# Optimization experiments

Hardware: AMD Instinct MI355X
Metric: run time of the kernel (lower is better)

## Reference

```python
import jax, jax.numpy as jnp
import numpy as np

S = 1024      # flattened hierarchical sequence length
D = 1024      # n_embd
H = 16        # n_head
HD = D // H   # head dim (64)
NL = 6        # n_layer
DFF = 4 * D
EPS = 1.1920929e-07  # torch rms_norm default eps (float32 machine eps)


def setup_inputs() -> dict:
    key = jax.random.key(0)
    ks = jax.random.split(key, 12)
    s = 0.02
    return {
        "x": jax.random.normal(ks[0], (1, S, D), jnp.float32),
        "Wq": jax.random.normal(ks[1], (NL, D, D), jnp.float32) * s,
        "Wk": jax.random.normal(ks[2], (NL, D, D), jnp.float32) * s,
        "Wv": jax.random.normal(ks[3], (NL, D, D), jnp.float32) * s,
        "Wo": jax.random.normal(ks[4], (NL, D, D), jnp.float32) * s,
        "lamb": jnp.full((NL,), 0.5, jnp.float32),
        "lambdas": jnp.tile(jnp.array([1.0, 0.0], jnp.float32), (NL, 1)),
        "Wfc": jax.random.normal(ks[5], (NL, DFF, D), jnp.float32) * s,
        "Wp": jax.random.normal(ks[6], (NL, D, DFF), jnp.float32) * s,
        "levels": jax.random.randint(ks[7], (S,), 0, 3, jnp.int32),
        "sample_idx": jnp.sort(jax.random.randint(ks[8], (S,), 0, 8, jnp.int32)),
    }


def rms(t):
    return t * jax.lax.rsqrt(jnp.mean(t * t, axis=-1, keepdims=True) + EPS)


def rope(t):
    # t: [B, T, H, hd]; torch-style half-split rotary
    hd = t.shape[-1]
    d = hd // 2
    inv = 1.0 / (10000.0 ** (jnp.arange(0, hd, 2, dtype=jnp.float32) / hd))
    fr = jnp.outer(jnp.arange(t.shape[1], dtype=jnp.float32), inv)  # [T, d]
    cos = jnp.cos(fr)[None, :, None, :]
    sin = jnp.sin(fr)[None, :, None, :]
    x1, x2 = t[..., :d], t[..., d:]
    return jnp.concatenate([x1 * cos + x2 * sin, -x1 * sin + x2 * cos], axis=-1)


def markov_mask(levels, sample_idx):
    # allowed(q,kv) = causal & same-sample & NOT(levels[kv]==0 and a level-0
    # token exists strictly between kv and q). Equivalent to the torch
    # markov_causal_mask, computed via a cumsum instead of torch.any.
    n = levels.shape[0]
    pos = jnp.arange(n)
    causal = pos[:, None] >= pos[None, :]
    same = sample_idx[:, None] == sample_idx[None, :]
    c = jnp.cumsum((levels == 0).astype(jnp.int32))
    cpad = jnp.concatenate([jnp.zeros((1,), jnp.int32), c])  # cpad[i]=#l0 in [0,i)
    # count of level-0 tokens at positions p with kv < p < q
    cnt = cpad[pos[:, None]] - cpad[pos[None, :] + 1]
    markov = (levels[None, :] == 0) & (cnt > 0)
    return causal & same & ~markov


def reference(x, Wq, Wk, Wv, Wo, lamb, lambdas, Wfc, Wp, levels, sample_idx):
    mask = markov_mask(levels, sample_idx)[None, None]  # [1,1,S,S]
    scale = HD ** -0.5
    neg = jnp.float32(-1e30)

    x = rms(x)          # norm of the hierarchical-trajectory embedding
    x0 = x
    v1 = None
    for i in range(NL):
        xl = lambdas[i, 0] * x + lambdas[i, 1] * x0
        xn = rms(xl)
        B, T = xn.shape[0], xn.shape[1]
        q = (xn @ Wq[i].T).reshape(B, T, H, HD)
        k = (xn @ Wk[i].T).reshape(B, T, H, HD)
        v = (xn @ Wv[i].T).reshape(B, T, H, HD)
        if v1 is None:
            v1 = v
        v = (1.0 - lamb[i]) * v + lamb[i] * v1   # value residual
        q, k = rms(q), rms(k)                    # QK RMSNorm
        q, k = rope(q), rope(k)
        scores = jnp.einsum("bqhd,bkhd->bhqk", q, k) * scale
        scores = jnp.where(mask, scores, neg)
        p = jax.nn.softmax(scores, axis=-1)
        y = jnp.einsum("bhqk,bkhd->bqhd", p, v).reshape(B, T, D)
        x = xl + y @ Wo[i].T
        h = rms(x) @ Wfc[i].T
        h = jnp.square(jax.nn.relu(h))           # relu(x)^2 activation
        x = x + h @ Wp[i].T
    return rms(x)
```

## Files before the change

kernel.cpp:

```cpp
#include <hip/hip_runtime.h>

#define SQ 1024
#define DM 1024
#define NH 16
#define HD 64
#define NL 6
#define DFF 4096
#define EPS 1.1920929e-07f

typedef __attribute__((ext_vector_type(8))) short short8;
typedef __attribute__((ext_vector_type(4))) float floatx4;
typedef __attribute__((address_space(1))) const unsigned int GU32;
typedef __attribute__((address_space(3))) unsigned int LU32;

__device__ __forceinline__ unsigned short f2b(float f) {
    union { float f; unsigned int u; } x; x.f = f;
    unsigned int r = x.u + 0x7fffu + ((x.u >> 16) & 1u);
    return (unsigned short)(r >> 16);
}

__device__ __forceinline__ float wsum(float v) {
#pragma unroll
    for (int m = 32; m >= 1; m >>= 1) v += __shfl_xor(v, m, 64);
    return v;
}
__device__ __forceinline__ float bsum(float v) {
    __shared__ float sh[4];
    v = wsum(v);
    __syncthreads();
    if ((threadIdx.x & 63) == 0) sh[threadIdx.x >> 6] = v;
    __syncthreads();
    return sh[0] + sh[1] + sh[2] + sh[3];
}

__global__ void convert_all(const float* __restrict__ s0, const float* __restrict__ s1,
                            const float* __restrict__ s2, const float* __restrict__ s3,
                            const float* __restrict__ s4, const float* __restrict__ s5,
                            unsigned short* __restrict__ d0, unsigned short* __restrict__ d1,
                            unsigned short* __restrict__ d2, unsigned short* __restrict__ d3,
                            unsigned short* __restrict__ d4, unsigned short* __restrict__ d5) {
    int bid = blockIdx.x;
    const float* src; unsigned short* dst; long base;
    if (bid < 1536)        { src = s0; dst = d0; base = (long)bid * 512; }
    else if (bid < 3072)   { src = s1; dst = d1; base = (long)(bid - 1536) * 512; }
    else if (bid < 4608)   { src = s2; dst = d2; base = (long)(bid - 3072) * 512; }
    else if (bid < 6144)   { src = s3; dst = d3; base = (long)(bid - 4608) * 512; }
    else if (bid < 12288)  { src = s4; dst = d4; base = (long)(bid - 6144) * 512; }
    else                   { src = s5; dst = d5; base = (long)(bid - 12288) * 512; }
    long i0 = base + threadIdx.x;
#pragma unroll
    for (int u = 0; u < 2; ++u) {
        long i = i0 + u * 256;
        float4 a = ((const float4*)src)[2 * i];
        float4 b = ((const float4*)src)[2 * i + 1];
        short8 o;
        o[0] = (short)f2b(a.x); o[1] = (short)f2b(a.y);
        o[2] = (short)f2b(a.z); o[3] = (short)f2b(a.w);
        o[4] = (short)f2b(b.x); o[5] = (short)f2b(b.y);
        o[6] = (short)f2b(b.z); o[7] = (short)f2b(b.w);
        *(short8*)(dst + i * 8) = o;
    }
}

__global__ void build_rope(float2* __restrict__ tab) {
    int i = blockIdx.x * 256 + threadIdx.x;
    int s = i >> 5, d = i & 31;
    float invf = expf(-((float)(2 * d) / (float)HD) * 9.210340371976184f);
    float fr = (float)s * invf;
    tab[i] = make_float2(cosf(fr), sinf(fr));
}

__global__ void scan_levels(const int* __restrict__ levels, int* __restrict__ cpad) {
    __shared__ int sh[SQ];
    int t = threadIdx.x;
    sh[t] = (levels[t] == 0) ? 1 : 0;
    __syncthreads();
    for (int off = 1; off < SQ; off <<= 1) {
        int v = (t >= off) ? sh[t - off] : 0;
        __syncthreads();
        sh[t] += v;
        __syncthreads();
    }
    cpad[t + 1] = sh[t];
    if (t == 0) cpad[0] = 0;
}

__global__ void build_mask_bits(const int* __restrict__ levels, const int* __restrict__ sidx,
                                const int* __restrict__ cpad, unsigned long long* __restrict__ mb) {
    int i = blockIdx.x * 256 + threadIdx.x;
    int q = i >> 10, k = i & 1023;
    bool causal = q >= k;
    bool same = sidx[q] == sidx[k];
    int cnt = cpad[q] - cpad[k + 1];
    bool markov = (levels[k] == 0) && (cnt > 0);
    bool pred = causal && same && !markov;
    unsigned long long bal = __ballot(pred);
    if ((threadIdx.x & 63) == 0) mb[(size_t)q * 16 + (k >> 6)] = bal;
}

__global__ void rms0(const float* __restrict__ xin, const float* __restrict__ lam2,
                     float* __restrict__ x0, float* __restrict__ xl,
                     unsigned short* __restrict__ xnb) {
    int row = blockIdx.x, t = threadIdx.x;
    float l0 = lam2[0], l1 = lam2[1];
    const float* rp = xin + (size_t)row * DM;
    float v[4]; float ss = 0.f;
#pragma unroll
    for (int j = 0; j < 4; ++j) { v[j] = rp[t + j * 256]; ss += v[j] * v[j]; }
    ss = bsum(ss);
    float inv = rsqrtf(ss / (float)DM + EPS);
    float coef = l0 + l1;
    float w[4]; float ss2 = 0.f;
#pragma unroll
    for (int j = 0; j < 4; ++j) {
        float r = v[j] * inv;
        x0[(size_t)row * DM + t + j * 256] = r;
        w[j] = coef * r;
        ss2 += w[j] * w[j];
    }
    ss2 = bsum(ss2);
    float inv2 = rsqrtf(ss2 / (float)DM + EPS);
#pragma unroll
    for (int j = 0; j < 4; ++j) {
        size_t idx = (size_t)row * DM + t + j * 256;
        xl[idx] = w[j];
        xnb[idx] = f2b(w[j] * inv2);
    }
}

__global__ __launch_bounds__(256, 2)
void gemm_qkv(const unsigned short* __restrict__ A,
              const unsigned short* __restrict__ B0,
              long long sB,
              unsigned short* __restrict__ qb, unsigned short* __restrict__ kb,
              float* __restrict__ v1, unsigned short* __restrict__ vt,
              const float2* __restrict__ rope,
              const float* __restrict__ lambp, int first) {
    constexpr int BM = 64, BN = 128, BK = 64;
    __shared__ unsigned short As[BM * BK];
    __shared__ unsigned short Bs[BN * BK];
    __shared__ unsigned short vtile[128 * 72];
    int t = threadIdx.x, wave = t >> 6, lane = t & 63;
    int m0 = blockIdx.y * BM, n0 = blockIdx.x * BN;
    int z = blockIdx.z;
    const unsigned short* Bb = B0 + (size_t)z * sB;
    int r = lane & 15, q4 = lane >> 4;
    int sr8 = lane >> 3, sseg8 = lane & 7;
    int wmo = (wave >> 1) * 32, wno = (wave & 1) * 64;

    floatx4 acc[2][4] = {};

    for (int k0 = 0; k0 < DM; k0 += BK) {
#pragma unroll
        for (int j = 0; j < 2; ++j) {
            int c = wave * 2 + j;
            const unsigned short* g = A + (size_t)(m0 + c * 8 + sr8) * DM + k0 + sseg8 * 8;
            __builtin_amdgcn_global_load_lds((GU32*)g, (LU32*)(As + c * 512), 16, 0, 0);
        }
#pragma unroll
        for (int j = 0; j < 4; ++j) {
            int c = wave * 4 + j;
            const unsigned short* g = Bb + (size_t)(n0 + c * 8 + sr8) * DM + k0 + sseg8 * 8;
            __builtin_amdgcn_global_load_lds((GU32*)g, (LU32*)(Bs + c * 512), 16, 0, 0);
        }
        __syncthreads();
#pragma unroll
        for (int kk = 0; kk < 2; ++kk) {
            short8 af[2], bfr[4];
#pragma unroll
            for (int mi = 0; mi < 2; ++mi)
                af[mi] = *(const short8*)(As + (wmo + mi * 16 + r) * BK + kk * 32 + q4 * 8);
#pragma unroll
            for (int ni = 0; ni < 4; ++ni)
                bfr[ni] = *(const short8*)(Bs + (wno + ni * 16 + r) * BK + kk * 32 + q4 * 8);
#pragma unroll
            for (int mi = 0; mi < 2; ++mi)
#pragma unroll
                for (int ni = 0; ni < 4; ++ni)
                    acc[mi][ni] = __builtin_amdgcn_mfma_f32_16x16x32_bf16(af[mi], bfr[ni], acc[mi][ni], 0, 0, 0);
        }
        __syncthreads();
    }

    if (z == 2) {
        float l = lambp[0];
#pragma unroll
        for (int mi = 0; mi < 2; ++mi)
#pragma unroll
            for (int ni = 0; ni < 4; ++ni)
#pragma unroll
                for (int j = 0; j < 4; ++j) {
                    int row = m0 + wmo + mi * 16 + q4 * 4 + j;
                    int col = n0 + wno + ni * 16 + r;
                    float val = acc[mi][ni][j];
                    size_t gi = (size_t)row * DM + col;
                    float v1v;
                    if (first) { v1[gi] = val; v1v = val; } else v1v = v1[gi];
                    vtile[(col - n0) * 72 + (row - m0)] = f2b((1.f - l) * val + l * v1v);
                }
        __syncthreads();
#pragma unroll
        for (int jj = 0; jj < 4; ++jj) {
            int idx = jj * 256 + t;
            int cr = idx >> 3;
            int seg = idx & 7;
            short8 o = *(const short8*)(&vtile[cr * 72 + seg * 8]);
            *(short8*)(vt + (size_t)(n0 + cr) * SQ + m0 + seg * 8) = o;
        }
        return;
    }

    unsigned short* dst = z ? kb : qb;
#pragma unroll
    for (int mi = 0; mi < 2; ++mi) {
#pragma unroll
        for (int j = 0; j < 4; ++j) {
            int row = m0 + wmo + mi * 16 + q4 * 4 + j;
            float v0 = acc[mi][0][j], v1x = acc[mi][1][j], v2 = acc[mi][2][j], v3 = acc[mi][3][j];
            float ss = v0 * v0 + v1x * v1x + v2 * v2 + v3 * v3;
#pragma unroll
            for (int d = 1; d < 16; d <<= 1) ss += __shfl_xor(ss, d, 64);
            float inv = rsqrtf(ss * (1.f / 64.f) + EPS);
            v0 *= inv; v1x *= inv; v2 *= inv; v3 *= inv;
            float2 t0 = rope[row * 32 + r];
            float2 t1 = rope[row * 32 + 16 + r];
            size_t rb = (size_t)row * DM + n0 + wno + r;
            dst[rb]      = f2b(v0 * t0.x + v2 * t0.y);
            dst[rb + 16] = f2b(v1x * t1.x + v3 * t1.y);
            dst[rb + 32] = f2b(v2 * t0.x - v0 * t0.y);
            dst[rb + 48] = f2b(v3 * t1.x - v1x * t1.y);
        }
    }
}

__global__ __launch_bounds__(64)
void flash_attn(const unsigned short* __restrict__ qb, const unsigned short* __restrict__ kb,
                const unsigned short* __restrict__ vt, const unsigned long long* __restrict__ mb,
                unsigned short* __restrict__ yb) {
    __shared__ unsigned short Ps[16 * 64];
    int lane = threadIdx.x;
    int qt = blockIdx.x & 63, h = blockIdx.x >> 6;
    int q0 = qt * 16;
    int r = lane & 15, q4 = lane >> 4;
    const unsigned short* qp = qb + (size_t)(q0 + r) * DM + h * HD + q4 * 8;
    short8 aq0 = *(const short8*)qp;
    short8 aq1 = *(const short8*)(qp + 32);
    floatx4 o[4] = {};
    float m[4] = {-1e30f, -1e30f, -1e30f, -1e30f};
    float l[4] = {0.f, 0.f, 0.f, 0.f};
    int nk = (qt >> 2) + 1;
    for (int kt = 0; kt < nk; ++kt) {
        int k0 = kt * 64;
        unsigned long long mw[4];
#pragma unroll
        for (int j = 0; j < 4; ++j) mw[j] = mb[(size_t)(q0 + q4 * 4 + j) * 16 + kt];
        unsigned long long any = mw[0] | mw[1] | mw[2] | mw[3];
        if (__ballot(any != 0ull) == 0ull) continue;
        short8 bk[4][2], bv[4][2];
#pragma unroll
        for (int ni = 0; ni < 4; ++ni) {
            const unsigned short* kp = kb + (size_t)(k0 + ni * 16 + r) * DM + h * HD + q4 * 8;
            bk[ni][0] = *(const short8*)kp;
            bk[ni][1] = *(const short8*)(kp + 32);
            const unsigned short* vp = vt + (size_t)(h * HD + ni * 16 + r) * SQ + k0 + q4 * 8;
            bv[ni][0] = *(const short8*)vp;
            bv[ni][1] = *(const short8*)(vp + 32);
        }
        float sm[4][4];
#pragma unroll
        for (int ni = 0; ni < 4; ++ni) {
            floatx4 z = {};
            z = __builtin_amdgcn_mfma_f32_16x16x32_bf16(aq0, bk[ni][0], z, 0, 0, 0);
            z = __builtin_amdgcn_mfma_f32_16x16x32_bf16(aq1, bk[ni][1], z, 0, 0, 0);
#pragma unroll
            for (int j = 0; j < 4; ++j) {
                float sv = z[j] * 0.125f;
                bool bit = (mw[j] >> (ni * 16 + r)) & 1ull;
                sm[ni][j] = bit ? sv : -__builtin_inff();
            }
        }
        float alpha[4];
#pragma unroll
        for (int j = 0; j < 4; ++j) {
            float v = fmaxf(fmaxf(sm[0][j], sm[1][j]), fmaxf(sm[2][j], sm[3][j]));
#pragma unroll
            for (int d = 1; d < 16; d <<= 1) v = fmaxf(v, __shfl_xor(v, d, 64));
            float mn = fmaxf(m[j], v);
            alpha[j] = __expf(m[j] - mn);
            m[j] = mn;
        }
        float p[4][4];
        float rs[4] = {0.f, 0.f, 0.f, 0.f};
#pragma unroll
        for (int ni = 0; ni < 4; ++ni)
#pragma unroll
            for (int j = 0; j < 4; ++j) {
                p[ni][j] = __expf(sm[ni][j] - m[j]);
                rs[j] += p[ni][j];
            }
#pragma unroll
        for (int j = 0; j < 4; ++j) {
            float v = rs[j];
#pragma unroll
            for (int d = 1; d < 16; d <<= 1) v += __shfl_xor(v, d, 64);
            l[j] = l[j] * alpha[j] + v;
        }
#pragma unroll
        for (int ni = 0; ni < 4; ++ni)
#pragma unroll
            for (int j = 0; j < 4; ++j) {
                o[ni][j] *= alpha[j];
                Ps[(q4 * 4 + j) * 64 + ni * 16 + r] = f2b(p[ni][j]);
            }
        short8 ap0 = *(const short8*)(Ps + r * 64 + q4 * 8);
        short8 ap1 = *(const short8*)(Ps + r * 64 + 32 + q4 * 8);
#pragma unroll
        for (int ni = 0; ni < 4; ++ni) {
            o[ni] = __builtin_amdgcn_mfma_f32_16x16x32_bf16(ap0, bv[ni][0], o[ni], 0, 0, 0);
            o[ni] = __builtin_amdgcn_mfma_f32_16x16x32_bf16(ap1, bv[ni][1], o[ni], 0, 0, 0);
        }
    }
#pragma unroll
    for (int j = 0; j < 4; ++j) l[j] = 1.f / l[j];
#pragma unroll
    for (int ni = 0; ni < 4; ++ni)
#pragma unroll
        for (int j = 0; j < 4; ++j)
            yb[(size_t)(q0 + q4 * 4 + j) * DM + h * HD + ni * 16 + r] = f2b(o[ni][j] * l[j]);
}

template<int BM, int BN>
__global__ __launch_bounds__(256, 2)
void gemm_t(const unsigned short* __restrict__ A, int lda, long long sA,
            const unsigned short* __restrict__ B, int ldb, long long sB,
            float* Cf, unsigned short* Cb, int ldc, long long sC,
            const float* __restrict__ addsrc, int ldadd,
            int K, float scale, int act) {
    constexpr int BK = 64;
    constexpr int MI = BM / 32, NI = BN / 32;
    constexpr int CAW = BM / 32, CBW = BN / 32;
    __shared__ unsigned short As[BM * BK];
    __shared__ unsigned short Bs[BN * BK];

    int t = threadIdx.x;
    int wave = t >> 6, lane = t & 63;
    int m0 = blockIdx.y * BM, n0 = blockIdx.x * BN;
    int z = blockIdx.z;
    const unsigned short* Ab = A + (size_t)z * sA;
    const unsigned short* Bb = B + (size_t)z * sB;

    int r = lane & 15, q4 = lane >> 4;
    int sr8 = lane >> 3, sseg8 = lane & 7;
    int wmo = (wave >> 1) * (BM / 2);
    int wno = (wave & 1) * (BN / 2);

    floatx4 acc[MI][NI] = {};

    for (int k0 = 0; k0 < K; k0 += BK) {
#pragma unroll
        for (int j = 0; j < CAW; ++j) {
            int c = wave * CAW + j;
            const unsigned short* g = Ab + (size_t)(m0 + c * 8 + sr8) * lda + k0 + sseg8 * 8;
            __builtin_amdgcn_global_load_lds((GU32*)g, (LU32*)(As + c * 512), 16, 0, 0);
        }
#pragma unroll
        for (int j = 0; j < CBW; ++j) {
            int c = wave * CBW + j;
            const unsigned short* g = Bb + (size_t)(n0 + c * 8 + sr8) * ldb + k0 + sseg8 * 8;
            __builtin_amdgcn_global_load_lds((GU32*)g, (LU32*)(Bs + c * 512), 16, 0, 0);
        }
        __syncthreads();
#pragma unroll
        for (int kk = 0; kk < 2; ++kk) {
            short8 af[MI], bfr[NI];
#pragma unroll
            for (int mi = 0; mi < MI; ++mi)
                af[mi] = *(const short8*)(As + (wmo + mi * 16 + r) * BK + kk * 32 + q4 * 8);
#pragma unroll
            for (int ni = 0; ni < NI; ++ni)
                bfr[ni] = *(const short8*)(Bs + (wno + ni * 16 + r) * BK + kk * 32 + q4 * 8);
#pragma unroll
            for (int mi = 0; mi < MI; ++mi)
#pragma unroll
                for (int ni = 0; ni < NI; ++ni)
                    acc[mi][ni] = __builtin_amdgcn_mfma_f32_16x16x32_bf16(af[mi], bfr[ni], acc[mi][ni], 0, 0, 0);
        }
        __syncthreads();
    }

    size_t cz = (size_t)z * sC;
#pragma unroll
    for (int mi = 0; mi < MI; ++mi) {
#pragma unroll
        for (int ni = 0; ni < NI; ++ni) {
            int col = n0 + wno + ni * 16 + r;
#pragma unroll
            for (int j = 0; j < 4; ++j) {
                int row = m0 + wmo + mi * 16 + q4 * 4 + j;
                float v = acc[mi][ni][j] * scale;
                if (addsrc) v += addsrc[(size_t)row * ldadd + col];
                if (act == 1) { v = fmaxf(v, 0.f); v = v * v; }
                if (Cf) Cf[cz + (size_t)row * ldc + col] = v;
                if (Cb) Cb[cz + (size_t)row * ldc + col] = f2b(v);
            }
        }
    }
}

__global__ void wo_rms(const float* __restrict__ xl, const float* __restrict__ pp,
                       float* __restrict__ x, unsigned short* __restrict__ xhb) {
    int row = blockIdx.x, t = threadIdx.x;
    const long n = (long)SQ * DM;
    size_t base = (size_t)row * DM;
    float a[4]; float ss = 0.f;
#pragma unroll
    for (int j = 0; j < 4; ++j) {
        size_t idx = base + t + j * 256;
        float v = xl[idx] + pp[idx] + pp[idx + n];
        x[idx] = v;
        a[j] = v; ss += v * v;
    }
    ss = bsum(ss);
    float inv = rsqrtf(ss / (float)DM + EPS);
#pragma unroll
    for (int j = 0; j < 4; ++j)
        xhb[base + t + j * 256] = f2b(a[j] * inv);
}

__global__ void proj_reduce_xlrms(const float* __restrict__ x, const float* __restrict__ pp,
                                  const float* __restrict__ x0, const float* __restrict__ lam2,
                                  float* __restrict__ xl, unsigned short* __restrict__ xnb,
                                  float* __restrict__ out, int last) {
    int row = blockIdx.x, t = threadIdx.x;
    const long n = (long)SQ * DM;
    size_t base = (size_t)row * DM;
    float l0 = 0.f, l1 = 0.f;
    if (!last) { l0 = lam2[0]; l1 = lam2[1]; }
    float a[4]; float ss = 0.f;
#pragma unroll
    for (int j = 0; j < 4; ++j) {
        size_t idx = base + t + j * 256;
        float v = x[idx] + pp[idx] + pp[idx + n] + pp[idx + 2 * n] + pp[idx + 3 * n];
        if (!last) { v = l0 * v + l1 * x0[idx]; xl[idx] = v; }
        a[j] = v; ss += v * v;
    }
    ss = bsum(ss);
    float inv = rsqrtf(ss / (float)DM + EPS);
#pragma unroll
    for (int j = 0; j < 4; ++j) {
        size_t idx = base + t + j * 256;
        if (last) out[idx] = a[j] * inv;
        else xnb[idx] = f2b(a[j] * inv);
    }
}

extern "C" void kernel_launch(void* const* d_in, const int* in_sizes, int n_in,
                              void* d_out, int out_size, void* d_ws, size_t ws_size,
                              hipStream_t stream) {
    const float* x_in    = (const float*)d_in[0];
    const float* Wq      = (const float*)d_in[1];
    const float* Wk      = (const float*)d_in[2];
    const float* Wv      = (const float*)d_in[3];
    const float* Wo      = (const float*)d_in[4];
    const float* lamb    = (const float*)d_in[5];
    const float* lambdas = (const float*)d_in[6];
    const float* Wfc     = (const float*)d_in[7];
    const float* Wp      = (const float*)d_in[8];
    const int*   levels  = (const int*)d_in[9];
    const int*   sidx    = (const int*)d_in[10];
    float* out = (float*)d_out;

    char* ws = (char*)d_ws;
    size_t off = 0;
    auto alloc = [&](size_t b) { void* p = ws + off; off = (off + b + 255) & ~(size_t)255; return p; };

    unsigned short* wq_b  = (unsigned short*)alloc((size_t)NL * DM * DM * 2);
    unsigned short* wk_b  = (unsigned short*)alloc((size_t)NL * DM * DM * 2);
    unsigned short* wv_b  = (unsigned short*)alloc((size_t)NL * DM * DM * 2);
    unsigned short* wo_b  = (unsigned short*)alloc((size_t)NL * DM * DM * 2);
    unsigned short* wfc_b = (unsigned short*)alloc((size_t)NL * DFF * DM * 2);
    unsigned short* wp_b  = (unsigned short*)alloc((size_t)NL * DM * DFF * 2);
    int* cpad             = (int*)alloc((SQ + 1) * 4);
    unsigned long long* mb = (unsigned long long*)alloc((size_t)SQ * 16 * 8);
    float2* rope          = (float2*)alloc((size_t)SQ * 32 * 8);
    float* x    = (float*)alloc((size_t)SQ * DM * 4);
    float* x0   = (float*)alloc((size_t)SQ * DM * 4);
    float* xl   = (float*)alloc((size_t)SQ * DM * 4);
    float* v1   = (float*)alloc((size_t)SQ * DM * 4);
    float* pp   = (float*)alloc((size_t)4 * SQ * DM * 4);
    unsigned short* xn_b = (unsigned short*)alloc((size_t)SQ * DM * 2);
    unsigned short* qb   = (unsigned short*)alloc((size_t)SQ * DM * 2);
    unsigned short* kb   = (unsigned short*)alloc((size_t)SQ * DM * 2);
    unsigned short* vt   = (unsigned short*)alloc((size_t)SQ * DM * 2);
    unsigned short* y_b  = (unsigned short*)alloc((size_t)SQ * DM * 2);
    unsigned short* xh_b = (unsigned short*)alloc((size_t)SQ * DM * 2);
    unsigned short* h_b  = (unsigned short*)alloc((size_t)SQ * DFF * 2);

    if (off > ws_size) return;

    const long long WSTRIDE = (long long)NL * DM * DM;
    const long long XSTRIDE = (long long)SQ * DM;

    convert_all<<<18432, 256, 0, stream>>>(Wq, Wk, Wv, Wo, Wfc, Wp,
                                           wq_b, wk_b, wv_b, wo_b, wfc_b, wp_b);

    scan_levels<<<1, 1024, 0, stream>>>(levels, cpad);
    build_mask_bits<<<4096, 256, 0, stream>>>(levels, sidx, cpad, mb);
    build_rope<<<128, 256, 0, stream>>>(rope);

    rms0<<<SQ, 256, 0, stream>>>(x_in, lambdas, x0, xl, xn_b);

    for (int i = 0; i < NL; ++i) {
        gemm_qkv<<<dim3(8, 16, 3), 256, 0, stream>>>(
            xn_b, wq_b + (size_t)i * DM * DM, WSTRIDE, qb, kb, v1, vt, rope,
            lamb + i, (i == 0) ? 1 : 0);

        flash_attn<<<1024, 64, 0, stream>>>(qb, kb, vt, mb, y_b);

        gemm_t<64, 64><<<dim3(16, 16, 2), 256, 0, stream>>>(
            y_b, DM, 512, wo_b + (size_t)i * DM * DM, DM, 512,
            pp, nullptr, DM, XSTRIDE, nullptr, 0, 512, 1.f, 0);
        wo_rms<<<SQ, 256, 0, stream>>>(xl, pp, x, xh_b);

        gemm_t<128, 64><<<dim3(64, 8, 1), 256, 0, stream>>>(
            xh_b, DM, 0, wfc_b + (size_t)i * DFF * DM, DM, 0,
            nullptr, h_b, DFF, 0, nullptr, 0, DM, 1.f, 1);
        gemm_t<128, 64><<<dim3(16, 8, 4), 256, 0, stream>>>(
            h_b, DFF, 1024, wp_b + (size_t)i * DM * DFF, DFF, 1024,
            pp, nullptr, DM, XSTRIDE, nullptr, 0, 1024, 1.f, 0);
        proj_reduce_xlrms<<<SQ, 256, 0, stream>>>(
            x, pp, x0, (i < NL - 1) ? (lambdas + 2 * (i + 1)) : nullptr,
            xl, xn_b, out, (i == NL - 1) ? 1 : 0);
    }
}
```

Baseline: 1.007 ms.

## Fuse fp32-to-bf16 weight conversion into GEMM B-tile staging

Removes the upfront convert_all pass that cast every weight matrix to bf16 into workspace buffers. Each GEMM now reads fp32 weights directly, rounds them to bf16 in registers and writes them to shared memory. This saves a full read/write pass over all weights and the matching workspace. In exchange, each GEMM reads twice the weight bytes, loses the asynchronous global_load_lds path for B, and redoes the conversion once per M-tile block.

```diff
diff --git a/kernel.cpp b/kernel.cpp
--- a/kernel.cpp
+++ b/kernel.cpp
@@ -31,35 +31,6 @@
     if ((threadIdx.x & 63) == 0) sh[threadIdx.x >> 6] = v;
     __syncthreads();
     return sh[0] + sh[1] + sh[2] + sh[3];
-}
-
-__global__ void convert_all(const float* __restrict__ s0, const float* __restrict__ s1,
-                            const float* __restrict__ s2, const float* __restrict__ s3,
-                            const float* __restrict__ s4, const float* __restrict__ s5,
-                            unsigned short* __restrict__ d0, unsigned short* __restrict__ d1,
-                            unsigned short* __restrict__ d2, unsigned short* __restrict__ d3,
-                            unsigned short* __restrict__ d4, unsigned short* __restrict__ d5) {
-    int bid = blockIdx.x;
-    const float* src; unsigned short* dst; long base;
-    if (bid < 1536)        { src = s0; dst = d0; base = (long)bid * 512; }
-    else if (bid < 3072)   { src = s1; dst = d1; base = (long)(bid - 1536) * 512; }
-    else if (bid < 4608)   { src = s2; dst = d2; base = (long)(bid - 3072) * 512; }
-    else if (bid < 6144)   { src = s3; dst = d3; base = (long)(bid - 4608) * 512; }
-    else if (bid < 12288)  { src = s4; dst = d4; base = (long)(bid - 6144) * 512; }
-    else                   { src = s5; dst = d5; base = (long)(bid - 12288) * 512; }
-    long i0 = base + threadIdx.x;
-#pragma unroll
-    for (int u = 0; u < 2; ++u) {
-        long i = i0 + u * 256;
-        float4 a = ((const float4*)src)[2 * i];
-        float4 b = ((const float4*)src)[2 * i + 1];
-        short8 o;
-        o[0] = (short)f2b(a.x); o[1] = (short)f2b(a.y);
-        o[2] = (short)f2b(a.z); o[3] = (short)f2b(a.w);
-        o[4] = (short)f2b(b.x); o[5] = (short)f2b(b.y);
-        o[6] = (short)f2b(b.z); o[7] = (short)f2b(b.w);
-        *(short8*)(dst + i * 8) = o;
-    }
 }
 
 __global__ void build_rope(float2* __restrict__ tab) {
@@ -128,10 +99,30 @@
     }
 }
 
+template<int BN>
+__device__ __forceinline__ void stage_b_f32(const float* __restrict__ Bf, int ldb,
+                                            int n0, int k0, int t,
+                                            unsigned short* __restrict__ Bs) {
+#pragma unroll
+    for (int p = 0; p < BN / 32; ++p) {
+        int row = p * 32 + (t >> 3);
+        int c8 = (t & 7) * 8;
+        const float* bg = Bf + (size_t)(n0 + row) * ldb + k0 + c8;
+        float4 u = *(const float4*)bg;
+        float4 w = *(const float4*)(bg + 4);
+        short8 ov;
+        ov[0] = (short)f2b(u.x); ov[1] = (short)f2b(u.y);
+        ov[2] = (short)f2b(u.z); ov[3] = (short)f2b(u.w);
+        ov[4] = (short)f2b(w.x); ov[5] = (short)f2b(w.y);
+        ov[6] = (short)f2b(w.z); ov[7] = (short)f2b(w.w);
+        *(short8*)(&Bs[row * 64 + c8]) = ov;
+    }
+}
+
 __global__ __launch_bounds__(256, 2)
 void gemm_qkv(const unsigned short* __restrict__ A,
-              const unsigned short* __restrict__ B0,
-              long long sB,
+              const float* __restrict__ WqL, const float* __restrict__ WkL,
+              const float* __restrict__ WvL,
               unsigned short* __restrict__ qb, unsigned short* __restrict__ kb,
               float* __restrict__ v1, unsigned short* __restrict__ vt,
               const float2* __restrict__ rope,
@@ -143,7 +134,7 @@
     int t = threadIdx.x, wave = t >> 6, lane = t & 63;
     int m0 = blockIdx.y * BM, n0 = blockIdx.x * BN;
     int z = blockIdx.z;
-    const unsigned short* Bb = B0 + (size_t)z * sB;
+    const float* Bf = (z == 0) ? WqL : (z == 1) ? WkL : WvL;
     int r = lane & 15, q4 = lane >> 4;
     int sr8 = lane >> 3, sseg8 = lane & 7;
     int wmo = (wave >> 1) * 32, wno = (wave & 1) * 64;
@@ -157,12 +148,7 @@
             const unsigned short* g = A + (size_t)(m0 + c * 8 + sr8) * DM + k0 + sseg8 * 8;
             __builtin_amdgcn_global_load_lds((GU32*)g, (LU32*)(As + c * 512), 16, 0, 0);
         }
-#pragma unroll
-        for (int j = 0; j < 4; ++j) {
-            int c = wave * 4 + j;
-            const unsigned short* g = Bb + (size_t)(n0 + c * 8 + sr8) * DM + k0 + sseg8 * 8;
-            __builtin_amdgcn_global_load_lds((GU32*)g, (LU32*)(Bs + c * 512), 16, 0, 0);
-        }
+        stage_b_f32<BN>(Bf, DM, n0, k0, t, Bs);
         __syncthreads();
 #pragma unroll
         for (int kk = 0; kk < 2; ++kk) {
@@ -332,13 +318,13 @@
 template<int BM, int BN>
 __global__ __launch_bounds__(256, 2)
 void gemm_t(const unsigned short* __restrict__ A, int lda, long long sA,
-            const unsigned short* __restrict__ B, int ldb, long long sB,
+            const float* __restrict__ B, int ldb, long long sB,
             float* Cf, unsigned short* Cb, int ldc, long long sC,
             const float* __restrict__ addsrc, int ldadd,
             int K, float scale, int act) {
     constexpr int BK = 64;
     constexpr int MI = BM / 32, NI = BN / 32;
-    constexpr int CAW = BM / 32, CBW = BN / 32;
+    constexpr int CAW = BM / 32;
     __shared__ unsigned short As[BM * BK];
     __shared__ unsigned short Bs[BN * BK];
 
@@ -347,7 +333,7 @@
     int m0 = blockIdx.y * BM, n0 = blockIdx.x * BN;
     int z = blockIdx.z;
     const unsigned short* Ab = A + (size_t)z * sA;
-    const unsigned short* Bb = B + (size_t)z * sB;
+    const float* Bb = B + (size_t)z * sB;
 
     int r = lane & 15, q4 = lane >> 4;
     int sr8 = lane >> 3, sseg8 = lane & 7;
@@ -363,12 +349,7 @@
             const unsigned short* g = Ab + (size_t)(m0 + c * 8 + sr8) * lda + k0 + sseg8 * 8;
             __builtin_amdgcn_global_load_lds((GU32*)g, (LU32*)(As + c * 512), 16, 0, 0);
         }
-#pragma unroll
-        for (int j = 0; j < CBW; ++j) {
-            int c = wave * CBW + j;
-            const unsigned short* g = Bb + (size_t)(n0 + c * 8 + sr8) * ldb + k0 + sseg8 * 8;
-            __builtin_amdgcn_global_load_lds((GU32*)g, (LU32*)(Bs + c * 512), 16, 0, 0);
-        }
+        stage_b_f32<BN>(Bb, ldb, n0, k0, t, Bs);
         __syncthreads();
 #pragma unroll
         for (int kk = 0; kk < 2; ++kk) {
@@ -474,12 +455,6 @@
     size_t off = 0;
     auto alloc = [&](size_t b) { void* p = ws + off; off = (off + b + 255) & ~(size_t)255; return p; };
 
-    unsigned short* wq_b  = (unsigned short*)alloc((size_t)NL * DM * DM * 2);
-    unsigned short* wk_b  = (unsigned short*)alloc((size_t)NL * DM * DM * 2);
-    unsigned short* wv_b  = (unsigned short*)alloc((size_t)NL * DM * DM * 2);
-    unsigned short* wo_b  = (unsigned short*)alloc((size_t)NL * DM * DM * 2);
-    unsigned short* wfc_b = (unsigned short*)alloc((size_t)NL * DFF * DM * 2);
-    unsigned short* wp_b  = (unsigned short*)alloc((size_t)NL * DM * DFF * 2);
     int* cpad             = (int*)alloc((SQ + 1) * 4);
     unsigned long long* mb = (unsigned long long*)alloc((size_t)SQ * 16 * 8);
     float2* rope          = (float2*)alloc((size_t)SQ * 32 * 8);
@@ -498,11 +473,7 @@
 
     if (off > ws_size) return;
 
-    const long long WSTRIDE = (long long)NL * DM * DM;
     const long long XSTRIDE = (long long)SQ * DM;
-
-    convert_all<<<18432, 256, 0, stream>>>(Wq, Wk, Wv, Wo, Wfc, Wp,
-                                           wq_b, wk_b, wv_b, wo_b, wfc_b, wp_b);
 
     scan_levels<<<1, 1024, 0, stream>>>(levels, cpad);
     build_mask_bits<<<4096, 256, 0, stream>>>(levels, sidx, cpad, mb);
@@ -511,22 +482,25 @@
     rms0<<<SQ, 256, 0, stream>>>(x_in, lambdas, x0, xl, xn_b);
 
     for (int i = 0; i < NL; ++i) {
+        size_t wo4 = (size_t)i * DM * DM;
+        size_t wf4 = (size_t)i * DFF * DM;
+
         gemm_qkv<<<dim3(8, 16, 3), 256, 0, stream>>>(
-            xn_b, wq_b + (size_t)i * DM * DM, WSTRIDE, qb, kb, v1, vt, rope,
+            xn_b, Wq + wo4, Wk + wo4, Wv + wo4, qb, kb, v1, vt, rope,
             lamb + i, (i == 0) ? 1 : 0);
 
         flash_attn<<<1024, 64, 0, stream>>>(qb, kb, vt, mb, y_b);
 
         gemm_t<64, 64><<<dim3(16, 16, 2), 256, 0, stream>>>(
-            y_b, DM, 512, wo_b + (size_t)i * DM * DM, DM, 512,
+            y_b, DM, 512, Wo + wo4, DM, 512,
             pp, nullptr, DM, XSTRIDE, nullptr, 0, 512, 1.f, 0);
         wo_rms<<<SQ, 256, 0, stream>>>(xl, pp, x, xh_b);
 
         gemm_t<128, 64><<<dim3(64, 8, 1), 256, 0, stream>>>(
-            xh_b, DM, 0, wfc_b + (size_t)i * DFF * DM, DM, 0,
+            xh_b, DM, 0, Wfc + wf4, DM, 0,
             nullptr, h_b, DFF, 0, nullptr, 0, DM, 1.f, 1);
         gemm_t<128, 64><<<dim3(16, 8, 4), 256, 0, stream>>>(
-            h_b, DFF, 1024, wp_b + (size_t)i * DM * DFF, DFF, 1024,
+            h_b, DFF, 1024, Wp + wf4, DFF, 1024,
             pp, nullptr, DM, XSTRIDE, nullptr, 0, 1024, 1.f, 0);
         proj_reduce_xlrms<<<SQ, 256, 0, stream>>>(
             x, pp, x0, (i < NL - 1) ? (lambdas + 2 * (i + 1)) : nullptr,
```

Measured after the change: 1.202 ms. 19.4% more time.
